# Kernel optimization log

Hardware: AMD Instinct MI355X
Metric: run time of the kernel (lower is better)

Reference implementation:

```python
import jax, jax.numpy as jnp
import numpy as np

N = 100000   # nodes
E = 800000   # edges (avg degree 8)
IN = 128     # in_dim
H = 128      # hidden_dim
L = 3        # num_layers
EPS = 1e-5   # torch LayerNorm default


def setup_inputs() -> dict:
    key = jax.random.key(0)
    ks = jax.random.split(key, 10)
    s = 0.05
    # DAG edge list: src < dst guarantees acyclicity and node N-1 is a sink.
    rng = np.random.default_rng(0)
    src = rng.integers(0, N - 1, size=E)
    dst = src + 1 + (rng.random(E) * (N - 1 - src)).astype(np.int64)
    return {
        "node_feats": jax.random.normal(ks[0], (N, IN), jnp.float32),
        "src": jnp.asarray(src, jnp.int32),
        "dst": jnp.asarray(dst, jnp.int32),
        "W_in": jax.random.normal(ks[1], (IN, H), jnp.float32) * s,
        "b_in": jnp.zeros((H,), jnp.float32),
        "Ws": jax.random.normal(ks[2], (L, H, H), jnp.float32) * s,
        "bs": jnp.zeros((L, H), jnp.float32),
        "Wn": jax.random.normal(ks[3], (L, H, H), jnp.float32) * s,
        "bn": jnp.zeros((L, H), jnp.float32),
        "Wg": jax.random.normal(ks[4], (L, 2 * H, H), jnp.float32) * s,
        "bg": jnp.zeros((L, H), jnp.float32),
        "gamma": jnp.ones((L, H), jnp.float32),
        "beta": jnp.zeros((L, H), jnp.float32),
        "W_att": jax.random.normal(ks[5], (H, H), jnp.float32) * s,
        "b_att": jnp.zeros((H,), jnp.float32),
        "W_score": jax.random.normal(ks[6], (H, 1), jnp.float32) * s,
        "b_score": jnp.zeros((1,), jnp.float32),
    }


def reference(node_feats, src, dst, W_in, b_in, Ws, bs, Wn, bn, Wg, bg,
              gamma, beta, W_att, b_att, W_score, b_score):
    n = node_feats.shape[0]
    ones_e = jnp.ones(src.shape, node_feats.dtype)
    indeg = jax.ops.segment_sum(ones_e, dst, num_segments=n)          # [N]
    has_pred = (indeg > 0).astype(node_feats.dtype)[:, None]          # [N,1]
    inv_deg = (1.0 / jnp.maximum(indeg, 1.0))[:, None]                # [N,1]
    outdeg = jax.ops.segment_sum(ones_e, src, num_segments=n)
    sink_mask = outdeg == 0                                           # [N]

    h = node_feats @ W_in + b_in                                      # [N,H]
    for i in range(Ws.shape[0]):
        hs = h @ Ws[i] + bs[i]
        # predecessor mean of layer-input h (no within-layer recurrence)
        neigh = jax.ops.segment_sum(h[src], dst, num_segments=n) * inv_deg
        hn = neigh @ Wn[i] + bn[i]
        m = hs + has_pred * hn  # nodes with no preds use m = hs only (bias too)
        gate = jax.nn.sigmoid(jnp.concatenate([h, m], axis=-1) @ Wg[i] + bg[i])
        v = gate * m + (1.0 - gate) * h
        mu = v.mean(-1, keepdims=True)
        var = ((v - mu) ** 2).mean(-1, keepdims=True)
        v = (v - mu) * jax.lax.rsqrt(var + EPS) * gamma[i] + beta[i]
        h = jax.nn.relu(v)

    # attention pooling over sink nodes only
    a = jnp.tanh(h @ W_att + b_att)
    scores = (a @ W_score)[:, 0] + b_score[0]
    scores = jnp.where(sink_mask, scores, -jnp.inf)
    w = jax.nn.softmax(scores, axis=0)  # zero weight on non-sinks
    graph_emb = (w[:, None] * h).sum(0)
    return h, graph_emb
```

## Files before the change

kernel.cpp:

```cpp
#include <hip/hip_runtime.h>
#include <cmath>

typedef unsigned short u16;
typedef unsigned int   u32;
typedef __attribute__((ext_vector_type(8))) short bf16x8;
typedef __attribute__((ext_vector_type(4))) float f32x4;
typedef __attribute__((ext_vector_type(4))) u32   u32x4;

__device__ __forceinline__ float bf2f(u16 u){
    union { u32 i; float f; } x; x.i = ((u32)u) << 16; return x.f;
}
__device__ __forceinline__ u16 f2bf(float f){
    union { float f; u32 i; } x; x.f = f;
    u32 r = x.i + 0x7fffu + ((x.i >> 16) & 1u);
    return (u16)(r >> 16);
}


__global__ void k_count(const int* __restrict__ src, const int* __restrict__ dst,
                        int* cnt, int* notsink, int* pos, int E){
    int e = blockIdx.x*256 + threadIdx.x;
    if (e < E){
        pos[e] = atomicAdd(&cnt[dst[e]], 1);
        notsink[src[e]] = 1;
    }
}

__global__ void k_scan1(const int* __restrict__ in, int* blocksum, int N){
    __shared__ int sh[256];
    int tid = threadIdx.x;
    int base = blockIdx.x*1024 + tid*4;
    int s = 0;
    for (int j=0;j<4;j++){ int i = base+j; s += (i < N) ? in[i] : 0; }
    sh[tid] = s; __syncthreads();
    for (int d=128; d>0; d>>=1){ if (tid < d) sh[tid] += sh[tid+d]; __syncthreads(); }
    if (tid == 0) blocksum[blockIdx.x] = sh[0];
}

__global__ void k_scan2(int* blocksum, int nb){
    if (threadIdx.x == 0){
        int run = 0;
        for (int i=0;i<nb;i++){ int v = blocksum[i]; blocksum[i] = run; run += v; }
    }
}

__global__ void k_scan3(const int* __restrict__ in, const int* __restrict__ blockoff,
                        int* out, float* inv_deg, float* haspred, int N){
    __shared__ int sh[256];
    int tid = threadIdx.x;
    int base = blockIdx.x*1024 + tid*4;
    int e[4]; int s = 0;
    for (int j=0;j<4;j++){ int i = base+j; e[j] = (i < N) ? in[i] : 0; s += e[j]; }
    sh[tid] = s; __syncthreads();
    for (int d=1; d<256; d<<=1){
        int t = (tid >= d) ? sh[tid-d] : 0;
        __syncthreads();
        sh[tid] += t;
        __syncthreads();
    }
    int excl = sh[tid] - s + blockoff[blockIdx.x];
    for (int j=0;j<4;j++){
        int i = base+j;
        if (i < N){
            out[i] = excl; excl += e[j];
            inv_deg[i] = 1.0f / (float)(e[j] > 1 ? e[j] : 1);
            haspred[i] = e[j] > 0 ? 1.0f : 0.0f;
        }
    }
}

__global__ void k_place(const int* __restrict__ src, const int* __restrict__ dst,
                        const int* __restrict__ row_ptr, const int* __restrict__ pos,
                        int* csr_src, int E){
    int e = blockIdx.x*256 + threadIdx.x;
    if (e < E)
        csr_src[row_ptr[dst[e]] + pos[e]] = src[e];
}

__global__ void k_wt(const float* __restrict__ in, u16* __restrict__ out,
                     int shift, int K, int total){
    int i = blockIdx.x*256 + threadIdx.x;
    if (i < total){
        int mat = i >> shift;
        int within = i & ((1 << shift) - 1);
        int k = within >> 7, n = within & 127;
        out[(size_t)mat*(K*128) + n*K + k] = f2bf(in[i]);
    }
}


__global__ void k_neigh(const u16* __restrict__ h, const int* __restrict__ row_ptr,
                        const int* __restrict__ indeg, const float* __restrict__ inv_deg,
                        const int* __restrict__ csr_src, u16* __restrict__ neigh, int N){
    int wid  = (blockIdx.x*256 + threadIdx.x) >> 6;
    int lane = threadIdx.x & 63;
    int sub = lane >> 4, sl = lane & 15;
    int node = wid*4 + sub;
    bool valid = node < N;
    int deg   = valid ? indeg[node]   : 0;
    int start = valid ? row_ptr[node] : 0;
    float acc[8] = {0.f,0.f,0.f,0.f,0.f,0.f,0.f,0.f};
    for (int e0 = 0; __any(e0 < deg); e0 += 16){
        int idx = 0;
        if (e0 + sl < deg) idx = csr_src[start + e0 + sl];
        int cnt = deg - e0;
        #pragma unroll
        for (int j = 0; j < 16; j++){
            int sidx = __shfl(idx, (sub << 4) | j);
            if (j < cnt){
                bf16x8 v = *(const bf16x8*)(h + (size_t)sidx*128 + sl*8);
                #pragma unroll
                for (int t=0;t<8;t++) acc[t] += bf2f((u16)v[t]);
            }
        }
    }
    if (valid){
        float iv = inv_deg[node];
        u16 o[8];
        #pragma unroll
        for (int t=0;t<8;t++) o[t] = f2bf(acc[t]*iv);
        *(u32x4*)(neigh + (size_t)node*128 + sl*8) = *(const u32x4*)o;
    }
}


__device__ __forceinline__ void stage_A_bf16(const u16* __restrict__ A, u16 (*lA)[136],
                                             int row0, int n_rows, int tid){
    #pragma unroll
    for (int i=0;i<4;i++){
        int c = i*256 + tid;
        int r = c >> 4, col8 = (c & 15) * 8;
        u32x4 v = {0,0,0,0};
        if (row0 + r < n_rows)
            v = *(const u32x4*)(A + (size_t)(row0 + r)*128 + col8);
        *(u32x4*)&lA[r][col8] = v;
    }
}

__device__ __forceinline__ void stage_A_f32(const float* __restrict__ A, u16 (*lA)[136],
                                            int row0, int n_rows, int tid){
    #pragma unroll
    for (int i=0;i<4;i++){
        int c = i*256 + tid;
        int r = c >> 4, col8 = (c & 15) * 8;
        u16 o[8] = {0,0,0,0,0,0,0,0};
        if (row0 + r < n_rows){
            float4 v0 = *(const float4*)(A + (size_t)(row0 + r)*128 + col8);
            float4 v1 = *(const float4*)(A + (size_t)(row0 + r)*128 + col8 + 4);
            o[0]=f2bf(v0.x); o[1]=f2bf(v0.y); o[2]=f2bf(v0.z); o[3]=f2bf(v0.w);
            o[4]=f2bf(v1.x); o[5]=f2bf(v1.y); o[6]=f2bf(v1.z); o[7]=f2bf(v1.w);
        }
        *(u32x4*)&lA[r][col8] = *(const u32x4*)o;
    }
}

__device__ __forceinline__ void stage_B(const u16* __restrict__ BT, int Ks, int koff0,
                                        u16 (*lB)[136], int tid){
    #pragma unroll
    for (int i=0;i<8;i++){
        int c = i*256 + tid;
        int n = c >> 4, col8 = (c & 15) * 8;
        u32x4 v = *(const u32x4*)(BT + (size_t)n*Ks + koff0 + col8);
        *(u32x4*)&lB[n][col8] = v;
    }
}

__device__ __forceinline__ void stage_B_half(const u16* __restrict__ BT, int Ks, int koff0,
                                             u16 (*lB)[72], int tid){
    #pragma unroll
    for (int i=0;i<4;i++){
        int c = i*256 + tid;
        int n = c >> 3, col8 = (c & 7) * 8;
        *(u32x4*)&lB[n][col8] = *(const u32x4*)(BT + (size_t)n*Ks + koff0 + col8);
    }
}

__device__ __forceinline__ void mfma_tile(const u16 (*lA)[136], const u16 (*lB)[136],
                                          int wave, int lane, f32x4* acc){
    #pragma unroll
    for (int kk=0;kk<4;kk++){
        int koff = kk*32 + (lane >> 4) * 8;
        bf16x8 a = *(const bf16x8*)&lA[wave*16 + (lane & 15)][koff];
        #pragma unroll
        for (int t=0;t<8;t++){
            bf16x8 b = *(const bf16x8*)&lB[t*16 + (lane & 15)][koff];
            acc[t] = __builtin_amdgcn_mfma_f32_16x16x32_bf16(a, b, acc[t], 0, 0, 0);
        }
    }
}

__device__ __forceinline__ void mfma_half(const u16 (*lA)[136], const u16 (*lB)[72],
                                          int wave, int lane, int kbaseA, f32x4* acc){
    #pragma unroll
    for (int kk=0;kk<2;kk++){
        int kw = kk*32 + (lane >> 4) * 8;
        bf16x8 a = *(const bf16x8*)&lA[wave*16 + (lane & 15)][kbaseA + kw];
        #pragma unroll
        for (int t=0;t<8;t++){
            bf16x8 b = *(const bf16x8*)&lB[t*16 + (lane & 15)][kw];
            acc[t] = __builtin_amdgcn_mfma_f32_16x16x32_bf16(a, b, acc[t], 0, 0, 0);
        }
    }
}


__global__ __launch_bounds__(256) void k_gemm_in(
    const float* __restrict__ A, const u16* __restrict__ BT,
    const float* __restrict__ bias, u16* __restrict__ C, int n_rows)
{
    __shared__ u16 lA[64][136];
    __shared__ u16 lB[128][136];
    int tid = threadIdx.x, wave = tid >> 6, lane = tid & 63;
    int row0 = blockIdx.x * 64;
    f32x4 acc[8];
    #pragma unroll
    for (int t=0;t<8;t++) acc[t] = (f32x4){0.f,0.f,0.f,0.f};
    stage_A_f32(A, lA, row0, n_rows, tid);
    stage_B(BT, 128, 0, lB, tid);
    __syncthreads();
    mfma_tile(lA, lB, wave, lane, acc);

    int sl = lane & 15;
    int rbase = wave*16 + (lane >> 4)*4;
    float bc[8];
    #pragma unroll
    for (int t=0;t<8;t++) bc[t] = bias[t*16 + sl];
    for (int r=0;r<4;r++){
        int row = row0 + rbase + r;
        if (row >= n_rows) continue;
        #pragma unroll
        for (int t=0;t<8;t++)
            C[(size_t)row*128 + t*16 + sl] = f2bf(acc[t][r] + bc[t]);
    }
}


__global__ __launch_bounds__(256) void k_layer(
    const u16* __restrict__ H, const u16* __restrict__ Ng,
    const u16* __restrict__ BsT, const u16* __restrict__ BnT,
    const u16* __restrict__ BgT,
    const float* __restrict__ bs, const float* __restrict__ bn,
    const float* __restrict__ bg,
    const float* __restrict__ gamma, const float* __restrict__ beta,
    const float* __restrict__ haspred,
    u16* __restrict__ Hb, float* __restrict__ Hf, int n_rows)
{
    __shared__ u16 lA[64][136];
    __shared__ u16 lM[64][136];
    __shared__ u16 lB[128][72];
    int tid = threadIdx.x, wave = tid >> 6, lane = tid & 63;
    int sl = lane & 15;
    int row0 = blockIdx.x * 64;
    f32x4 accs[8], accn[8];
    #pragma unroll
    for (int t=0;t<8;t++){ accs[t] = (f32x4){0.f,0.f,0.f,0.f}; accn[t] = (f32x4){0.f,0.f,0.f,0.f}; }

    stage_A_bf16(H, lA, row0, n_rows, tid);
    stage_B_half(BsT, 128, 0, lB, tid);
    __syncthreads();
    mfma_half(lA, lB, wave, lane, 0, accs);
    __syncthreads();
    stage_B_half(BsT, 128, 64, lB, tid);
    __syncthreads();
    mfma_half(lA, lB, wave, lane, 64, accs);
    __syncthreads();

    stage_A_bf16(Ng, lM, row0, n_rows, tid);
    stage_B_half(BnT, 128, 0, lB, tid);
    __syncthreads();
    mfma_half(lM, lB, wave, lane, 0, accn);
    __syncthreads();
    stage_B_half(BnT, 128, 64, lB, tid);
    __syncthreads();
    mfma_half(lM, lB, wave, lane, 64, accn);
    __syncthreads();

    int rbase = wave*16 + (lane >> 4)*4;
    {
        float bsc[8], bnc[8];
        #pragma unroll
        for (int t=0;t<8;t++){ bsc[t] = bs[t*16 + sl]; bnc[t] = bn[t*16 + sl]; }
        #pragma unroll
        for (int r=0;r<4;r++){
            int row = row0 + rbase + r;
            float hp = (row < n_rows) ? haspred[row] : 0.f;
            #pragma unroll
            for (int t=0;t<8;t++){
                float m = accs[t][r] + bsc[t] + hp*(accn[t][r] + bnc[t]);
                lM[rbase + r][t*16 + sl] = f2bf(m);
            }
        }
    }
    __syncthreads();

    #pragma unroll
    for (int t=0;t<8;t++) accs[t] = (f32x4){0.f,0.f,0.f,0.f};
    stage_B_half(BgT, 256, 0, lB, tid);
    __syncthreads();
    mfma_half(lA, lB, wave, lane, 0, accs);
    __syncthreads();
    stage_B_half(BgT, 256, 64, lB, tid);
    __syncthreads();
    mfma_half(lA, lB, wave, lane, 64, accs);
    __syncthreads();
    stage_B_half(BgT, 256, 128, lB, tid);
    __syncthreads();
    mfma_half(lM, lB, wave, lane, 0, accs);
    __syncthreads();
    stage_B_half(BgT, 256, 192, lB, tid);
    __syncthreads();
    mfma_half(lM, lB, wave, lane, 64, accs);
    __syncthreads();

    float bgc[8], gam[8], bet[8];
    #pragma unroll
    for (int t=0;t<8;t++){
        int col = t*16 + sl;
        bgc[t] = bg[col]; gam[t] = gamma[col]; bet[t] = beta[col];
    }
    for (int r=0;r<4;r++){
        int row = row0 + rbase + r;
        if (row >= n_rows) continue;
        float v[8], s = 0.f;
        #pragma unroll
        for (int t=0;t<8;t++){
            int col = t*16 + sl;
            float x = accs[t][r] + bgc[t];
            float g = 1.f/(1.f + expf(-x));
            float hv = bf2f(H[(size_t)row*128 + col]);
            float mv = bf2f(lM[rbase + r][col]);
            v[t] = g*mv + (1.f - g)*hv;
            s += v[t];
        }
        s += __shfl_xor(s,1); s += __shfl_xor(s,2); s += __shfl_xor(s,4); s += __shfl_xor(s,8);
        float mu = s * (1.f/128.f);
        float q = 0.f;
        #pragma unroll
        for (int t=0;t<8;t++){ float d = v[t]-mu; q += d*d; }
        q += __shfl_xor(q,1); q += __shfl_xor(q,2); q += __shfl_xor(q,4); q += __shfl_xor(q,8);
        float rs = rsqrtf(q*(1.f/128.f) + 1e-5f);
        #pragma unroll
        for (int t=0;t<8;t++){
            size_t idx = (size_t)row*128 + t*16 + sl;
            float o = (v[t]-mu)*rs*gam[t] + bet[t];
            o = o > 0.f ? o : 0.f;
            Hb[idx] = f2bf(o);
            if (Hf) Hf[idx] = o;
        }
    }
}


__global__ __launch_bounds__(256) void k_gemm_att(
    const u16* __restrict__ H, const u16* __restrict__ BT,
    const float* __restrict__ b_att, const float* __restrict__ Wsc,
    const float* __restrict__ bsc, const int* __restrict__ notsink,
    float* __restrict__ scores, int n_rows)
{
    __shared__ u16 lA[64][136];
    __shared__ u16 lB[128][136];
    int tid = threadIdx.x, wave = tid >> 6, lane = tid & 63;
    int row0 = blockIdx.x * 64;
    f32x4 acc[8];
    #pragma unroll
    for (int t=0;t<8;t++) acc[t] = (f32x4){0.f,0.f,0.f,0.f};
    stage_A_bf16(H, lA, row0, n_rows, tid);
    stage_B(BT, 128, 0, lB, tid);
    __syncthreads();
    mfma_tile(lA, lB, wave, lane, acc);

    int sl = lane & 15;
    int rbase = wave*16 + (lane >> 4)*4;
    float bac[8], wc[8];
    #pragma unroll
    for (int t=0;t<8;t++){ bac[t] = b_att[t*16 + sl]; wc[t] = Wsc[t*16 + sl]; }
    float b0 = bsc[0];
    for (int r=0;r<4;r++){
        int row = row0 + rbase + r;
        if (row >= n_rows) continue;
        float p = 0.f;
        #pragma unroll
        for (int t=0;t<8;t++) p += tanhf(acc[t][r] + bac[t]) * wc[t];
        p += __shfl_xor(p,1); p += __shfl_xor(p,2); p += __shfl_xor(p,4); p += __shfl_xor(p,8);
        if (sl == 0)
            scores[row] = (notsink[row] == 0) ? (p + b0) : -INFINITY;
    }
}


__global__ void k_sum1(const float* __restrict__ scores, float* part, int N){
    __shared__ float sh[256];
    int tid = threadIdx.x;
    float s = 0.f;
    for (int i = blockIdx.x*256 + tid; i < N; i += 256*256) s += expf(scores[i]);
    sh[tid] = s; __syncthreads();
    for (int d=128; d>0; d>>=1){ if (tid < d) sh[tid] += sh[tid+d]; __syncthreads(); }
    if (tid == 0) part[blockIdx.x] = sh[0];
}

__global__ void k_sum2(const float* __restrict__ part, float* invsum){
    __shared__ float sh[256];
    int tid = threadIdx.x;
    sh[tid] = part[tid]; __syncthreads();
    for (int d=128; d>0; d>>=1){ if (tid < d) sh[tid] += sh[tid+d]; __syncthreads(); }
    if (tid == 0) invsum[0] = 1.f / sh[0];
}

__global__ void k_emb1(const u16* __restrict__ h, const float* __restrict__ scores,
                       float* accum, int N){
    __shared__ float sh[256];
    int tid = threadIdx.x;
    int col = tid & 127, grp = tid >> 7;
    float acc = 0.f;
    for (int n = blockIdx.x*2 + grp; n < N; n += 512){
        float s = scores[n];
        if (s > -1e30f){
            float w = expf(s);
            acc += w * bf2f(h[(size_t)n*128 + col]);
        }
    }
    sh[tid] = acc; __syncthreads();
    if (tid < 128) atomicAdd(&accum[col], sh[tid] + sh[tid+128]);
}

__global__ void k_emb2(const float* __restrict__ accum, const float* __restrict__ invsum,
                       float* __restrict__ out){
    int c = threadIdx.x;
    if (c < 128) out[c] = accum[c] * invsum[0];
}


extern "C" void kernel_launch(void* const* d_in, const int* in_sizes, int n_in,
                              void* d_out, int out_size, void* d_ws, size_t ws_size,
                              hipStream_t stream)
{
    const float* node_feats = (const float*)d_in[0];
    const int* src     = (const int*)d_in[1];
    const int* dst     = (const int*)d_in[2];
    const float* W_in    = (const float*)d_in[3];
    const float* b_in    = (const float*)d_in[4];
    const float* Ws      = (const float*)d_in[5];
    const float* bs      = (const float*)d_in[6];
    const float* Wn      = (const float*)d_in[7];
    const float* bn      = (const float*)d_in[8];
    const float* Wg      = (const float*)d_in[9];
    const float* bg      = (const float*)d_in[10];
    const float* gamma   = (const float*)d_in[11];
    const float* beta    = (const float*)d_in[12];
    const float* W_att   = (const float*)d_in[13];
    const float* b_att   = (const float*)d_in[14];
    const float* W_score = (const float*)d_in[15];
    const float* b_score = (const float*)d_in[16];

    const int N = in_sizes[0] / 128;
    const int E = in_sizes[1];

    char* w = (char*)d_ws;
    auto alloc = [&](size_t bytes)->char* {
        char* p = w; w += (bytes + 255) & ~(size_t)255; return p;
    };
    u16* WT_in  = (u16*)alloc(128*128*2);
    u16* WT_s   = (u16*)alloc(3*128*128*2);
    u16* WT_n   = (u16*)alloc(3*128*128*2);
    u16* WT_g   = (u16*)alloc(3*128*256*2);
    u16* WT_att = (u16*)alloc(128*128*2);
    int* cnt      = (int*)alloc((size_t)N*4);
    int* notsink  = (int*)alloc((size_t)N*4);
    float* emb_accum = (float*)alloc(128*4);
    size_t zero_bytes = (size_t)((char*)(emb_accum + 128) - (char*)cnt);
    int* pos      = (int*)alloc((size_t)E*4);
    int* row_ptr  = (int*)alloc((size_t)N*4);
    int* blocksum = (int*)alloc(1024*4);
    int* csr_src  = (int*)alloc((size_t)E*4);
    float* inv_deg = (float*)alloc((size_t)N*4);
    float* haspred = (float*)alloc((size_t)N*4);
    float* scores  = (float*)alloc((size_t)N*4);
    float* part    = (float*)alloc(256*4);
    float* invsum  = (float*)alloc(256);
    u16* buf_h = (u16*)alloc((size_t)N*128*2);
    u16* buf_b = (u16*)alloc((size_t)N*128*2);

    float* h_out   = (float*)d_out;
    float* emb_out = h_out + (size_t)N*128;

    hipMemsetAsync(cnt, 0, zero_bytes, stream);

    k_wt<<<(16384+255)/256, 256, 0, stream>>>(W_in,  WT_in,  14, 128, 16384);
    k_wt<<<(49152+255)/256, 256, 0, stream>>>(Ws,    WT_s,   14, 128, 49152);
    k_wt<<<(49152+255)/256, 256, 0, stream>>>(Wn,    WT_n,   14, 128, 49152);
    k_wt<<<(98304+255)/256, 256, 0, stream>>>(Wg,    WT_g,   15, 256, 98304);
    k_wt<<<(16384+255)/256, 256, 0, stream>>>(W_att, WT_att, 14, 128, 16384);

    k_count<<<(E+255)/256, 256, 0, stream>>>(src, dst, cnt, notsink, pos, E);

    int nb = (N + 1023) / 1024;
    k_scan1<<<nb, 256, 0, stream>>>(cnt, blocksum, N);
    k_scan2<<<1, 256, 0, stream>>>(blocksum, nb);
    k_scan3<<<nb, 256, 0, stream>>>(cnt, blocksum, row_ptr, inv_deg, haspred, N);
    k_place<<<(E+255)/256, 256, 0, stream>>>(src, dst, row_ptr, pos, csr_src, E);

    int gblk = (N + 63) / 64;
    int nblk = (N + 15) / 16;

    k_gemm_in<<<gblk, 256, 0, stream>>>(node_feats, WT_in, b_in, buf_h, N);

    for (int i=0;i<3;i++){
        k_neigh<<<nblk, 256, 0, stream>>>(buf_h, row_ptr, cnt, inv_deg, csr_src, buf_b, N);
        float* f32out = (i == 2) ? h_out : nullptr;
        k_layer<<<gblk, 256, 0, stream>>>(buf_h, buf_b,
                                          WT_s + i*16384, WT_n + i*16384, WT_g + i*32768,
                                          bs + i*128, bn + i*128, bg + i*128,
                                          gamma + i*128, beta + i*128, haspred,
                                          buf_h, f32out, N);
    }

    k_gemm_att<<<gblk, 256, 0, stream>>>(buf_h, WT_att, b_att, W_score, b_score,
                                         notsink, scores, N);
    k_sum1<<<256, 256, 0, stream>>>(scores, part, N);
    k_sum2<<<1, 256, 0, stream>>>(part, invsum);
    k_emb1<<<256, 256, 0, stream>>>(buf_h, scores, emb_accum, N);
    k_emb2<<<1, 128, 0, stream>>>(emb_accum, invsum, emb_out);

    (void)n_in; (void)out_size; (void)ws_size;
}
```

Before: 627.6 us.

## Fuse neighbor mean aggregation into layer kernel with ping-pong h buffers

Removes the separate k_neigh kernel and computes each block's 64 predecessor means directly into shared memory inside k_layer. This avoids writing and re-reading the neighbor buffer, and ping-pong buffers replace the in-place update to avoid a race with other blocks' gathers. The gate blend now reads h from shared memory instead of global. The final layer skips the bf16 store, so the attention and embedding kernels read the fp32 output instead. The gather runs with one node per 16 lanes inside a 256-thread block, which may hurt latency hiding and occupancy because of the large shared-memory footprint.

```diff
diff --git a/kernel.cpp b/kernel.cpp
--- a/kernel.cpp
+++ b/kernel.cpp
@@ -89,41 +89,6 @@
 }
 
 
-__global__ void k_neigh(const u16* __restrict__ h, const int* __restrict__ row_ptr,
-                        const int* __restrict__ indeg, const float* __restrict__ inv_deg,
-                        const int* __restrict__ csr_src, u16* __restrict__ neigh, int N){
-    int wid  = (blockIdx.x*256 + threadIdx.x) >> 6;
-    int lane = threadIdx.x & 63;
-    int sub = lane >> 4, sl = lane & 15;
-    int node = wid*4 + sub;
-    bool valid = node < N;
-    int deg   = valid ? indeg[node]   : 0;
-    int start = valid ? row_ptr[node] : 0;
-    float acc[8] = {0.f,0.f,0.f,0.f,0.f,0.f,0.f,0.f};
-    for (int e0 = 0; __any(e0 < deg); e0 += 16){
-        int idx = 0;
-        if (e0 + sl < deg) idx = csr_src[start + e0 + sl];
-        int cnt = deg - e0;
-        #pragma unroll
-        for (int j = 0; j < 16; j++){
-            int sidx = __shfl(idx, (sub << 4) | j);
-            if (j < cnt){
-                bf16x8 v = *(const bf16x8*)(h + (size_t)sidx*128 + sl*8);
-                #pragma unroll
-                for (int t=0;t<8;t++) acc[t] += bf2f((u16)v[t]);
-            }
-        }
-    }
-    if (valid){
-        float iv = inv_deg[node];
-        u16 o[8];
-        #pragma unroll
-        for (int t=0;t<8;t++) o[t] = f2bf(acc[t]*iv);
-        *(u32x4*)(neigh + (size_t)node*128 + sl*8) = *(const u32x4*)o;
-    }
-}
-
-
 __device__ __forceinline__ void stage_A_bf16(const u16* __restrict__ A, u16 (*lA)[136],
                                              int row0, int n_rows, int tid){
     #pragma unroll
@@ -236,7 +201,9 @@
 
 
 __global__ __launch_bounds__(256) void k_layer(
-    const u16* __restrict__ H, const u16* __restrict__ Ng,
+    const u16* __restrict__ H,
+    const int* __restrict__ row_ptr, const int* __restrict__ indeg,
+    const float* __restrict__ inv_deg, const int* __restrict__ csr_src,
     const u16* __restrict__ BsT, const u16* __restrict__ BnT,
     const u16* __restrict__ BgT,
     const float* __restrict__ bs, const float* __restrict__ bn,
@@ -249,13 +216,46 @@
     __shared__ u16 lM[64][136];
     __shared__ u16 lB[128][72];
     int tid = threadIdx.x, wave = tid >> 6, lane = tid & 63;
-    int sl = lane & 15;
+    int sl = lane & 15, g16 = lane >> 4;
     int row0 = blockIdx.x * 64;
+
+    stage_A_bf16(H, lA, row0, n_rows, tid);
+
+    #pragma unroll
+    for (int pass=0; pass<4; pass++){
+        int r = pass*16 + wave*4 + g16;
+        int node = row0 + r;
+        if (node < n_rows){
+            float acc[8] = {0.f,0.f,0.f,0.f,0.f,0.f,0.f,0.f};
+            int deg = indeg[node], start = row_ptr[node];
+            for (int e0 = 0; e0 < deg; e0 += 16){
+                int idx = (e0 + sl < deg) ? csr_src[start + e0 + sl] : 0;
+                int c = deg - e0;
+                #pragma unroll
+                for (int j = 0; j < 16; j++){
+                    int sidx = __shfl(idx, (g16 << 4) | j);
+                    if (j < c){
+                        bf16x8 v = *(const bf16x8*)(H + (size_t)sidx*128 + sl*8);
+                        #pragma unroll
+                        for (int t=0;t<8;t++) acc[t] += bf2f((u16)v[t]);
+                    }
+                }
+            }
+            float iv = inv_deg[node];
+            u16 o[8];
+            #pragma unroll
+            for (int t=0;t<8;t++) o[t] = f2bf(acc[t]*iv);
+            *(u32x4*)&lM[r][sl*8] = *(const u32x4*)o;
+        } else {
+            u32x4 z = {0,0,0,0};
+            *(u32x4*)&lM[r][sl*8] = z;
+        }
+    }
+
     f32x4 accs[8], accn[8];
     #pragma unroll
     for (int t=0;t<8;t++){ accs[t] = (f32x4){0.f,0.f,0.f,0.f}; accn[t] = (f32x4){0.f,0.f,0.f,0.f}; }
 
-    stage_A_bf16(H, lA, row0, n_rows, tid);
     stage_B_half(BsT, 128, 0, lB, tid);
     __syncthreads();
     mfma_half(lA, lB, wave, lane, 0, accs);
@@ -265,7 +265,6 @@
     mfma_half(lA, lB, wave, lane, 64, accs);
     __syncthreads();
 
-    stage_A_bf16(Ng, lM, row0, n_rows, tid);
     stage_B_half(BnT, 128, 0, lB, tid);
     __syncthreads();
     mfma_half(lM, lB, wave, lane, 0, accn);
@@ -275,7 +274,7 @@
     mfma_half(lM, lB, wave, lane, 64, accn);
     __syncthreads();
 
-    int rbase = wave*16 + (lane >> 4)*4;
+    int rbase = wave*16 + g16*4;
     {
         float bsc[8], bnc[8];
         #pragma unroll
@@ -326,10 +325,10 @@
         for (int t=0;t<8;t++){
             int col = t*16 + sl;
             float x = accs[t][r] + bgc[t];
-            float g = 1.f/(1.f + expf(-x));
-            float hv = bf2f(H[(size_t)row*128 + col]);
+            float gg = 1.f/(1.f + expf(-x));
+            float hv = bf2f(lA[rbase + r][col]);
             float mv = bf2f(lM[rbase + r][col]);
-            v[t] = g*mv + (1.f - g)*hv;
+            v[t] = gg*mv + (1.f - gg)*hv;
             s += v[t];
         }
         s += __shfl_xor(s,1); s += __shfl_xor(s,2); s += __shfl_xor(s,4); s += __shfl_xor(s,8);
@@ -344,7 +343,7 @@
             size_t idx = (size_t)row*128 + t*16 + sl;
             float o = (v[t]-mu)*rs*gam[t] + bet[t];
             o = o > 0.f ? o : 0.f;
-            Hb[idx] = f2bf(o);
+            if (Hb) Hb[idx] = f2bf(o);
             if (Hf) Hf[idx] = o;
         }
     }
@@ -352,7 +351,7 @@
 
 
 __global__ __launch_bounds__(256) void k_gemm_att(
-    const u16* __restrict__ H, const u16* __restrict__ BT,
+    const float* __restrict__ H, const u16* __restrict__ BT,
     const float* __restrict__ b_att, const float* __restrict__ Wsc,
     const float* __restrict__ bsc, const int* __restrict__ notsink,
     float* __restrict__ scores, int n_rows)
@@ -364,7 +363,7 @@
     f32x4 acc[8];
     #pragma unroll
     for (int t=0;t<8;t++) acc[t] = (f32x4){0.f,0.f,0.f,0.f};
-    stage_A_bf16(H, lA, row0, n_rows, tid);
+    stage_A_f32(H, lA, row0, n_rows, tid);
     stage_B(BT, 128, 0, lB, tid);
     __syncthreads();
     mfma_tile(lA, lB, wave, lane, acc);
@@ -406,7 +405,7 @@
     if (tid == 0) invsum[0] = 1.f / sh[0];
 }
 
-__global__ void k_emb1(const u16* __restrict__ h, const float* __restrict__ scores,
+__global__ void k_emb1(const float* __restrict__ h, const float* __restrict__ scores,
                        float* accum, int N){
     __shared__ float sh[256];
     int tid = threadIdx.x;
@@ -414,10 +413,8 @@
     float acc = 0.f;
     for (int n = blockIdx.x*2 + grp; n < N; n += 512){
         float s = scores[n];
-        if (s > -1e30f){
-            float w = expf(s);
-            acc += w * bf2f(h[(size_t)n*128 + col]);
-        }
+        if (s > -1e30f)
+            acc += expf(s) * h[(size_t)n*128 + col];
     }
     sh[tid] = acc; __syncthreads();
     if (tid < 128) atomicAdd(&accum[col], sh[tid] + sh[tid+128]);
@@ -477,8 +474,8 @@
     float* scores  = (float*)alloc((size_t)N*4);
     float* part    = (float*)alloc(256*4);
     float* invsum  = (float*)alloc(256);
-    u16* buf_h = (u16*)alloc((size_t)N*128*2);
-    u16* buf_b = (u16*)alloc((size_t)N*128*2);
+    u16* buf0 = (u16*)alloc((size_t)N*128*2);
+    u16* buf1 = (u16*)alloc((size_t)N*128*2);
 
     float* h_out   = (float*)d_out;
     float* emb_out = h_out + (size_t)N*128;
@@ -500,25 +497,26 @@
     k_place<<<(E+255)/256, 256, 0, stream>>>(src, dst, row_ptr, pos, csr_src, E);
 
     int gblk = (N + 63) / 64;
-    int nblk = (N + 15) / 16;
-
-    k_gemm_in<<<gblk, 256, 0, stream>>>(node_feats, WT_in, b_in, buf_h, N);
-
+
+    k_gemm_in<<<gblk, 256, 0, stream>>>(node_feats, WT_in, b_in, buf0, N);
+
+    u16* hin = buf0;
     for (int i=0;i<3;i++){
-        k_neigh<<<nblk, 256, 0, stream>>>(buf_h, row_ptr, cnt, inv_deg, csr_src, buf_b, N);
-        float* f32out = (i == 2) ? h_out : nullptr;
-        k_layer<<<gblk, 256, 0, stream>>>(buf_h, buf_b,
+        u16* hb  = (i == 2) ? nullptr : ((hin == buf0) ? buf1 : buf0);
+        float* hf = (i == 2) ? h_out : nullptr;
+        k_layer<<<gblk, 256, 0, stream>>>(hin, row_ptr, cnt, inv_deg, csr_src,
                                           WT_s + i*16384, WT_n + i*16384, WT_g + i*32768,
                                           bs + i*128, bn + i*128, bg + i*128,
                                           gamma + i*128, beta + i*128, haspred,
-                                          buf_h, f32out, N);
-    }
-
-    k_gemm_att<<<gblk, 256, 0, stream>>>(buf_h, WT_att, b_att, W_score, b_score,
+                                          hb, hf, N);
+        if (i < 2) hin = hb;
+    }
+
+    k_gemm_att<<<gblk, 256, 0, stream>>>(h_out, WT_att, b_att, W_score, b_score,
                                          notsink, scores, N);
     k_sum1<<<256, 256, 0, stream>>>(scores, part, N);
     k_sum2<<<1, 256, 0, stream>>>(part, invsum);
-    k_emb1<<<256, 256, 0, stream>>>(buf_h, scores, emb_accum, N);
+    k_emb1<<<256, 256, 0, stream>>>(h_out, scores, emb_accum, N);
     k_emb2<<<1, 128, 0, stream>>>(emb_accum, invsum, emb_out);
 
     (void)n_in; (void)out_size; (void)ws_size;
```

Measured after the change: 828.7 us. +32.1%, slower.
